# Kernel tuning notes

Hardware: AMD Instinct MI355X
Metric: run time of the kernel (lower is better)

## Reference

```python
import jax, jax.numpy as jnp
import numpy as np

N = 50000
E = 1600000
IN_F = 512
OUT_F = 128
NEG_SLOPE = 0.01   # nn.LeakyReLU() default
TEMPERATURE = 0.5


def setup_inputs() -> dict:
    key = jax.random.key(0)
    k1, k2, k3, k4 = jax.random.split(key, 4)
    h = jax.random.normal(k1, (N, IN_F), dtype=jnp.float32)
    # xavier_uniform with gain=1.414
    limW = 1.414 * np.sqrt(6.0 / (IN_F + OUT_F))
    W = jax.random.uniform(k2, (IN_F, OUT_F), minval=-limW, maxval=limW, dtype=jnp.float32)
    lima = 1.414 * np.sqrt(6.0 / (2 * OUT_F + 1))
    a = jax.random.uniform(k3, (2 * OUT_F, 1), minval=-lima, maxval=lima, dtype=jnp.float32)
    edge_index = jax.random.randint(k4, (2, E), 0, N, dtype=jnp.int64)
    return {"h": h, "W": W, "a": a, "edge_index": edge_index}


def reference(h, W, a, edge_index):
    # Inference: F.dropout(training=False) is identity.
    Wh = h @ W                                   # [N, F_out]
    src = edge_index[0]                          # row indices -> softmax segments
    dst = edge_index[1]
    # cat([Wh[src], Wh[dst]]) @ a == (Wh @ a1)[src] + (Wh @ a2)[dst]
    a1 = a[:OUT_F, 0]
    a2 = a[OUT_F:, 0]
    s1 = Wh @ a1                                 # [N]
    s2 = Wh @ a2                                 # [N]
    e = s1[src] + s2[dst]                        # [E]
    e = jnp.where(e >= 0, e, NEG_SLOPE * e)      # LeakyReLU
    logits = e / TEMPERATURE
    # sparse softmax over dim=1 (per source-node row segments)
    seg_max = jax.ops.segment_max(logits, src, num_segments=N)  # [N]
    ex = jnp.exp(logits - seg_max[src])          # [E]
    denom = jax.ops.segment_sum(ex, src, num_segments=N)        # [N]
    att = ex / denom[src]                        # [E]
    # sparse-dense matmul: h_prime[i] = sum_j att(i,j) * Wh[j]
    h_prime = jax.ops.segment_sum(att[:, None] * Wh[dst], src, num_segments=N)  # [N, F_out]
    return jax.nn.relu(h_prime)                  # concat=True path
```

## Files before the change

kernel.cpp:

```cpp
#include <hip/hip_runtime.h>
#include <cstdint>
#include <cstddef>

#define N_NODES 50000
#define N_EDGES 1600000
#define IN_FEAT 512
#define OUT_FEAT 128
#define NEG_SLOPE 0.01f
#define INV_TEMP 2.0f
#define PAD_DEG 128

#define BUCKETS 400
#define BNODES 125
#define BCAP 5000
#define A_BLOCKS 250
#define A_EPC (N_EDGES / A_BLOCKS)
#define A_G4 (A_EPC / 4)

#define CONV_BLOCKS ((IN_FEAT * OUT_FEAT) / 256)
#define GEMM_BLOCKS ((N_NODES + 63) / 64)

typedef __attribute__((ext_vector_type(8))) short short8;
typedef __attribute__((ext_vector_type(4))) float f32x4;

#define GLOBAL_AS __attribute__((address_space(1)))
#define LDS_AS __attribute__((address_space(3)))

__device__ inline unsigned short f2bf(float x) {
    unsigned int u = __float_as_uint(x);
    unsigned int r = (u + 0x7fffu + ((u >> 16) & 1u)) >> 16;
    return (unsigned short)r;
}
__device__ inline float bf2f(unsigned short b) {
    return __uint_as_float(((unsigned int)b) << 16);
}


__global__ __launch_bounds__(256) void build_kernel(const float* __restrict__ W,
                                                    unsigned short* __restrict__ Wt,
                                                    const int* __restrict__ src,
                                                    const int* __restrict__ dst,
                                                    int* __restrict__ bucket_cursor,
                                                    int* __restrict__ binned) {
    __shared__ int cntL[BUCKETS];
    __shared__ int baseL[BUCKETS];

    if (blockIdx.x >= A_BLOCKS) {
        int tid = (blockIdx.x - A_BLOCKS) * 256 + threadIdx.x;
        if (tid < IN_FEAT * OUT_FEAT) {
            int n = tid >> 9;
            int k = tid & 511;
            Wt[tid] = f2bf(W[k * OUT_FEAT + n]);
        }
        return;
    }

    int t = threadIdx.x;
    for (int i = t; i < BUCKETS; i += 256) cntL[i] = 0;
    __syncthreads();
    size_t ebase = (size_t)blockIdx.x * A_EPC;

    for (int g = t; g < A_G4; g += 256) {
        int4 s4 = *(const int4*)(src + ebase + (size_t)g * 4);
#pragma unroll
        for (int j = 0; j < 4; ++j) {
            int s = (&s4.x)[j];
            atomicAdd(&cntL[s / BNODES], 1);
        }
    }
    __syncthreads();
    for (int i = t; i < BUCKETS; i += 256) {
        int c = cntL[i];
        baseL[i] = c ? atomicAdd(&bucket_cursor[i], c) : 0;
        cntL[i] = 0;
    }
    __syncthreads();
    for (int g = t; g < A_G4; g += 256) {
        int4 s4 = *(const int4*)(src + ebase + (size_t)g * 4);
        int4 d4 = *(const int4*)(dst + ebase + (size_t)g * 4);
#pragma unroll
        for (int j = 0; j < 4; ++j) {
            int s = (&s4.x)[j];
            int b = s / BNODES;
            int sl = s - b * BNODES;
            int pos = atomicAdd(&cntL[b], 1);
            int slot = baseL[b] + pos;
            if (slot < BCAP)
                binned[(size_t)b * BCAP + slot] = (sl << 16) | (&d4.x)[j];
        }
    }
}


__global__ __launch_bounds__(256) void gemm_binB_kernel(const float* __restrict__ h,
                                                        const unsigned short* __restrict__ Wt,
                                                        const float* __restrict__ a_vec,
                                                        unsigned short* __restrict__ Whb,
                                                        float* __restrict__ s1,
                                                        float* __restrict__ s2,
                                                        const int* __restrict__ bucket_cursor,
                                                        const int* __restrict__ binned,
                                                        int* __restrict__ cnt,
                                                        int* __restrict__ csr) {
    __shared__ unsigned short lB[2][8 * 2 * 64 * 8];

    if (blockIdx.x < BUCKETS) {
        int* cL = (int*)&lB[0][0];
        int b = blockIdx.x;
        int t = threadIdx.x;
        if (t < BNODES) cL[t] = 0;
        __syncthreads();
        int m = min(bucket_cursor[b], BCAP);
        const int* bp = binned + (size_t)b * BCAP;
        int n0 = b * BNODES;
        for (int i = t; i < m; i += 256) {
            int p = bp[i];
            int sl = p >> 16;
            int d = p & 0xFFFF;
            int pos = atomicAdd(&cL[sl], 1);
            if (pos < PAD_DEG) csr[(size_t)(n0 + sl) * PAD_DEG + pos] = d;
        }
        __syncthreads();
        if (t < BNODES) cnt[n0 + t] = min(cL[t], PAD_DEG);
        return;
    }

    int bid = blockIdx.x - BUCKETS;
    int t = threadIdx.x;
    int w = t >> 6;
    int L = t & 63;
    int m0 = bid * 64;

    int arow = m0 + w * 16 + (L & 15);
    bool arow_ok = arow < N_NODES;
    int kq = (L >> 4) * 8;
    const float* arp = h + (size_t)arow * IN_FEAT + kq;

    f32x4 acc[8];
#pragma unroll
    for (int i = 0; i < 8; ++i) acc[i] = (f32x4){0.f, 0.f, 0.f, 0.f};

    auto stageB = [&](int buf, int k0) {
#pragma unroll
        for (int c = 0; c < 4; ++c) {
            int nb = w * 2 + (c >> 1);
            int ksub = c & 1;
            const GLOBAL_AS unsigned short* g =
                (const GLOBAL_AS unsigned short*)(Wt + (size_t)(nb * 16 + (L & 15)) * IN_FEAT +
                                                  (k0 + ksub * 32 + kq));
            LDS_AS unsigned short* lp = (LDS_AS unsigned short*)(&lB[buf][(nb * 2 + ksub) * 512]);
            __builtin_amdgcn_global_load_lds((const GLOBAL_AS void*)g, (LDS_AS void*)lp, 16, 0, 0);
        }
    };

    float4 av[2][2];
#pragma unroll
    for (int c = 0; c < 2; ++c) {
        av[c][0] = make_float4(0.f, 0.f, 0.f, 0.f);
        av[c][1] = make_float4(0.f, 0.f, 0.f, 0.f);
    }
    if (arow_ok) {
        av[0][0] = *(const float4*)(arp);
        av[0][1] = *(const float4*)(arp + 4);
        av[1][0] = *(const float4*)(arp + 32);
        av[1][1] = *(const float4*)(arp + 36);
    }
    stageB(0, 0);
    __syncthreads();

#pragma unroll
    for (int it = 0; it < 8; ++it) {
        const int buf = it & 1;

        if (it < 7) stageB(buf ^ 1, (it + 1) * 64);

        float4 avn[2][2];
#pragma unroll
        for (int c = 0; c < 2; ++c) {
            avn[c][0] = make_float4(0.f, 0.f, 0.f, 0.f);
            avn[c][1] = make_float4(0.f, 0.f, 0.f, 0.f);
        }
        if (it < 7 && arow_ok) {
            const float* p = arp + (it + 1) * 64;
            avn[0][0] = *(const float4*)(p);
            avn[0][1] = *(const float4*)(p + 4);
            avn[1][0] = *(const float4*)(p + 32);
            avn[1][1] = *(const float4*)(p + 36);
        }

        short8 af[2];
#pragma unroll
        for (int c = 0; c < 2; ++c) {
            short8 v;
            v[0] = (short)f2bf(av[c][0].x); v[1] = (short)f2bf(av[c][0].y);
            v[2] = (short)f2bf(av[c][0].z); v[3] = (short)f2bf(av[c][0].w);
            v[4] = (short)f2bf(av[c][1].x); v[5] = (short)f2bf(av[c][1].y);
            v[6] = (short)f2bf(av[c][1].z); v[7] = (short)f2bf(av[c][1].w);
            af[c] = v;
        }

#pragma unroll
        for (int ksub = 0; ksub < 2; ++ksub) {
#pragma unroll
            for (int nb = 0; nb < 8; ++nb) {
                short8 bf = *(const short8*)(&lB[buf][((nb * 2 + ksub) * 64 + L) * 8]);
                acc[nb] = __builtin_amdgcn_mfma_f32_16x16x32_bf16(af[ksub], bf, acc[nb], 0, 0, 0);
            }
        }

        __syncthreads();
#pragma unroll
        for (int c = 0; c < 2; ++c) {
            av[c][0] = avn[c][0];
            av[c][1] = avn[c][1];
        }
    }

    int col0 = L & 15;
    int rbase = m0 + w * 16 + (L >> 4) * 4;

    float a1c[8], a2c[8];
#pragma unroll
    for (int nb = 0; nb < 8; ++nb) {
        a1c[nb] = a_vec[nb * 16 + col0];
        a2c[nb] = a_vec[128 + nb * 16 + col0];
    }

#pragma unroll
    for (int r = 0; r < 4; ++r) {
        int row = rbase + r;
        bool ok = row < N_NODES;
        float p1 = 0.f, p2 = 0.f;
        if (ok) {
            unsigned short* orow = Whb + (size_t)row * OUT_FEAT;
#pragma unroll
            for (int nb = 0; nb < 8; ++nb) {
                float v = acc[nb][r];
                orow[nb * 16 + col0] = f2bf(v);
                p1 = fmaf(v, a1c[nb], p1);
                p2 = fmaf(v, a2c[nb], p2);
            }
        }
#pragma unroll
        for (int off = 8; off > 0; off >>= 1) {
            p1 += __shfl_xor(p1, off, 64);
            p2 += __shfl_xor(p2, off, 64);
        }
        if (ok && col0 == 0) {
            s1[row] = p1;
            s2[row] = p2;
        }
    }
}


__global__ __launch_bounds__(256) void node_kernel(const unsigned short* __restrict__ Whb,
                                                   const float* __restrict__ s1,
                                                   const float* __restrict__ s2,
                                                   const int* __restrict__ cnt,
                                                   const int* __restrict__ csr,
                                                   float* __restrict__ out) {
    int lane = threadIdx.x & 63;
    int w = threadIdx.x >> 6;
    int n = blockIdx.x * 4 + w;
    if (n >= N_NODES) return;
    int deg = cnt[n];
    size_t start = (size_t)n * PAD_DEG;
    int g = lane >> 4;
    int fo = lane & 15;

    float accv[8];
#pragma unroll
    for (int f = 0; f < 8; ++f) accv[f] = 0.f;
    float inv = 0.f;

    if (deg > 0) {
        float s1n = s1[n];
        int d0 = 0, d1 = 0;
        float ex0 = 0.f, ex1 = 0.f;
        if (lane < deg) {
            d0 = csr[start + lane];
            float ev = s1n + s2[d0];
            ev = ev >= 0.f ? ev : NEG_SLOPE * ev;
            ex0 = __expf(ev * INV_TEMP);
        }
        if (lane + 64 < deg) {
            d1 = csr[start + lane + 64];
            float ev = s1n + s2[d1];
            ev = ev >= 0.f ? ev : NEG_SLOPE * ev;
            ex1 = __expf(ev * INV_TEMP);
        }
        float denom = ex0 + ex1;
#pragma unroll
        for (int off = 32; off > 0; off >>= 1) denom += __shfl_xor(denom, off, 64);
        inv = 1.0f / denom;

#pragma unroll 2
        for (int jj = 0; jj < deg; jj += 4) {
            int e = jj + g;
            bool hi = jj >= 64;
            float exs = hi ? ex1 : ex0;
            int dsel = hi ? d1 : d0;
            float p = __shfl(exs, e & 63, 64);
            int dd = __shfl(dsel, e & 63, 64);
            short8 row = *(const short8*)(Whb + (size_t)dd * OUT_FEAT + fo * 8);
#pragma unroll
            for (int f = 0; f < 8; ++f)
                accv[f] = fmaf(p, bf2f((unsigned short)row[f]), accv[f]);
        }
#pragma unroll
        for (int f = 0; f < 8; ++f) {
            accv[f] += __shfl_xor(accv[f], 16, 64);
            accv[f] += __shfl_xor(accv[f], 32, 64);
        }
    }

    if (g == 0) {
        float* orow = out + (size_t)n * OUT_FEAT + fo * 8;
        float4 o0, o1;
        o0.x = fmaxf(accv[0] * inv, 0.f); o0.y = fmaxf(accv[1] * inv, 0.f);
        o0.z = fmaxf(accv[2] * inv, 0.f); o0.w = fmaxf(accv[3] * inv, 0.f);
        o1.x = fmaxf(accv[4] * inv, 0.f); o1.y = fmaxf(accv[5] * inv, 0.f);
        o1.z = fmaxf(accv[6] * inv, 0.f); o1.w = fmaxf(accv[7] * inv, 0.f);
        *(float4*)(orow) = o0;
        *(float4*)(orow + 4) = o1;
    }
}


extern "C" void kernel_launch(void* const* d_in, const int* in_sizes, int n_in,
                              void* d_out, int out_size, void* d_ws, size_t ws_size,
                              hipStream_t stream) {
    const float* h = (const float*)d_in[0];
    const float* W = (const float*)d_in[1];
    const float* a = (const float*)d_in[2];
    const int* edge = (const int*)d_in[3];
    const int* src = edge;
    const int* dst = edge + N_EDGES;
    float* out = (float*)d_out;

    char* ws = (char*)d_ws;
    size_t off = 0;
    auto alloc = [&](size_t bytes) -> void* {
        void* p = ws + off;
        off = (off + bytes + 255) & ~(size_t)255;
        return p;
    };
    unsigned short* Whb = (unsigned short*)alloc((size_t)N_NODES * OUT_FEAT * sizeof(unsigned short));
    float* s1 = (float*)alloc((size_t)N_NODES * sizeof(float));
    float* s2 = (float*)alloc((size_t)N_NODES * sizeof(float));
    int* cnt = (int*)alloc((size_t)N_NODES * sizeof(int));
    int* csr = (int*)alloc((size_t)N_NODES * PAD_DEG * sizeof(int));
    unsigned short* Wt = (unsigned short*)alloc((size_t)IN_FEAT * OUT_FEAT * sizeof(unsigned short));
    int* bucket_cursor = (int*)alloc((size_t)BUCKETS * sizeof(int));
    int* binned = (int*)alloc((size_t)BUCKETS * BCAP * sizeof(int));

    hipMemsetAsync(bucket_cursor, 0, BUCKETS * sizeof(int), stream);
    build_kernel<<<A_BLOCKS + CONV_BLOCKS, 256, 0, stream>>>(W, Wt, src, dst, bucket_cursor, binned);
    gemm_binB_kernel<<<BUCKETS + GEMM_BLOCKS, 256, 0, stream>>>(h, Wt, a, Whb, s1, s2,
                                                                bucket_cursor, binned, cnt, csr);
    node_kernel<<<(N_NODES + 3) / 4, 256, 0, stream>>>(Whb, s1, s2, cnt, csr, out);
}
```

Before: 262.8 us.

## Load GEMM B fragments directly to registers and double rows per wave

The GEMM part of the fused bin/gemm kernel no longer stages the bf16 weight tile into LDS through global_load_lds with double buffering and block barriers. Each wave now reads its B fragments straight from global memory (L2-resident, 128 KB) into registers and reuses them across two 16-row M tiles, so blocks cover 128 rows instead of 64. This removes the LDS traffic and the per-iteration __syncthreads and halves the GEMM block count. In exchange it raises register pressure (32 accumulators plus 16 B fragments) and repeats the global reads of W in every wave.

```diff
diff --git a/kernel.cpp b/kernel.cpp
--- a/kernel.cpp
+++ b/kernel.cpp
@@ -18,7 +18,7 @@
 #define A_G4 (A_EPC / 4)
 
 #define CONV_BLOCKS ((IN_FEAT * OUT_FEAT) / 256)
-#define GEMM_BLOCKS ((N_NODES + 63) / 64)
+#define GEMM_BLOCKS ((N_NODES + 127) / 128)
 
 typedef __attribute__((ext_vector_type(8))) short short8;
 typedef __attribute__((ext_vector_type(4))) float f32x4;
@@ -102,10 +102,9 @@
                                                         const int* __restrict__ binned,
                                                         int* __restrict__ cnt,
                                                         int* __restrict__ csr) {
-    __shared__ unsigned short lB[2][8 * 2 * 64 * 8];
+    __shared__ int cL[BNODES];
 
     if (blockIdx.x < BUCKETS) {
-        int* cL = (int*)&lB[0][0];
         int b = blockIdx.x;
         int t = threadIdx.x;
         if (t < BNODES) cL[t] = 0;
@@ -129,95 +128,109 @@
     int t = threadIdx.x;
     int w = t >> 6;
     int L = t & 63;
-    int m0 = bid * 64;
-
-    int arow = m0 + w * 16 + (L & 15);
-    bool arow_ok = arow < N_NODES;
+    int m0 = bid * 128;
+    int col0 = L & 15;
     int kq = (L >> 4) * 8;
-    const float* arp = h + (size_t)arow * IN_FEAT + kq;
-
-    f32x4 acc[8];
-#pragma unroll
-    for (int i = 0; i < 8; ++i) acc[i] = (f32x4){0.f, 0.f, 0.f, 0.f};
-
-    auto stageB = [&](int buf, int k0) {
-#pragma unroll
-        for (int c = 0; c < 4; ++c) {
-            int nb = w * 2 + (c >> 1);
-            int ksub = c & 1;
-            const GLOBAL_AS unsigned short* g =
-                (const GLOBAL_AS unsigned short*)(Wt + (size_t)(nb * 16 + (L & 15)) * IN_FEAT +
-                                                  (k0 + ksub * 32 + kq));
-            LDS_AS unsigned short* lp = (LDS_AS unsigned short*)(&lB[buf][(nb * 2 + ksub) * 512]);
-            __builtin_amdgcn_global_load_lds((const GLOBAL_AS void*)g, (LDS_AS void*)lp, 16, 0, 0);
-        }
-    };
-
-    float4 av[2][2];
-#pragma unroll
-    for (int c = 0; c < 2; ++c) {
-        av[c][0] = make_float4(0.f, 0.f, 0.f, 0.f);
-        av[c][1] = make_float4(0.f, 0.f, 0.f, 0.f);
-    }
-    if (arow_ok) {
-        av[0][0] = *(const float4*)(arp);
-        av[0][1] = *(const float4*)(arp + 4);
-        av[1][0] = *(const float4*)(arp + 32);
-        av[1][1] = *(const float4*)(arp + 36);
-    }
-    stageB(0, 0);
-    __syncthreads();
+
+    int arow[2];
+    bool arow_ok[2];
+    const float* arp[2];
+#pragma unroll
+    for (int m = 0; m < 2; ++m) {
+        arow[m] = m0 + w * 32 + m * 16 + col0;
+        arow_ok[m] = arow[m] < N_NODES;
+        arp[m] = h + (size_t)arow[m] * IN_FEAT + kq;
+    }
+
+    const unsigned short* bbase = Wt + (size_t)col0 * IN_FEAT + kq;
+
+    f32x4 acc[2][8];
+#pragma unroll
+    for (int m = 0; m < 2; ++m)
+#pragma unroll
+        for (int nb = 0; nb < 8; ++nb) acc[m][nb] = (f32x4){0.f, 0.f, 0.f, 0.f};
+
+    float4 av[2][2][2];
+#pragma unroll
+    for (int m = 0; m < 2; ++m)
+#pragma unroll
+        for (int c = 0; c < 2; ++c) {
+            av[m][c][0] = make_float4(0.f, 0.f, 0.f, 0.f);
+            av[m][c][1] = make_float4(0.f, 0.f, 0.f, 0.f);
+        }
+#pragma unroll
+    for (int m = 0; m < 2; ++m)
+        if (arow_ok[m]) {
+            av[m][0][0] = *(const float4*)(arp[m]);
+            av[m][0][1] = *(const float4*)(arp[m] + 4);
+            av[m][1][0] = *(const float4*)(arp[m] + 32);
+            av[m][1][1] = *(const float4*)(arp[m] + 36);
+        }
 
 #pragma unroll
     for (int it = 0; it < 8; ++it) {
-        const int buf = it & 1;
-
-        if (it < 7) stageB(buf ^ 1, (it + 1) * 64);
-
-        float4 avn[2][2];
-#pragma unroll
-        for (int c = 0; c < 2; ++c) {
-            avn[c][0] = make_float4(0.f, 0.f, 0.f, 0.f);
-            avn[c][1] = make_float4(0.f, 0.f, 0.f, 0.f);
-        }
-        if (it < 7 && arow_ok) {
-            const float* p = arp + (it + 1) * 64;
-            avn[0][0] = *(const float4*)(p);
-            avn[0][1] = *(const float4*)(p + 4);
-            avn[1][0] = *(const float4*)(p + 32);
-            avn[1][1] = *(const float4*)(p + 36);
-        }
-
-        short8 af[2];
-#pragma unroll
-        for (int c = 0; c < 2; ++c) {
-            short8 v;
-            v[0] = (short)f2bf(av[c][0].x); v[1] = (short)f2bf(av[c][0].y);
-            v[2] = (short)f2bf(av[c][0].z); v[3] = (short)f2bf(av[c][0].w);
-            v[4] = (short)f2bf(av[c][1].x); v[5] = (short)f2bf(av[c][1].y);
-            v[6] = (short)f2bf(av[c][1].z); v[7] = (short)f2bf(av[c][1].w);
-            af[c] = v;
-        }
-
-#pragma unroll
-        for (int ksub = 0; ksub < 2; ++ksub) {
+        const int k0 = it * 64;
+
+        float4 avn[2][2][2];
+#pragma unroll
+        for (int m = 0; m < 2; ++m)
+#pragma unroll
+            for (int c = 0; c < 2; ++c) {
+                avn[m][c][0] = make_float4(0.f, 0.f, 0.f, 0.f);
+                avn[m][c][1] = make_float4(0.f, 0.f, 0.f, 0.f);
+            }
+        if (it < 7) {
+#pragma unroll
+            for (int m = 0; m < 2; ++m)
+                if (arow_ok[m]) {
+                    const float* p = arp[m] + (it + 1) * 64;
+                    avn[m][0][0] = *(const float4*)(p);
+                    avn[m][0][1] = *(const float4*)(p + 4);
+                    avn[m][1][0] = *(const float4*)(p + 32);
+                    avn[m][1][1] = *(const float4*)(p + 36);
+                }
+        }
+
+        short8 bfr[2][8];
+#pragma unroll
+        for (int ksub = 0; ksub < 2; ++ksub)
+#pragma unroll
+            for (int nb = 0; nb < 8; ++nb)
+                bfr[ksub][nb] =
+                    *(const short8*)(bbase + (size_t)nb * 16 * IN_FEAT + k0 + ksub * 32);
+
+        short8 af[2][2];
+#pragma unroll
+        for (int m = 0; m < 2; ++m)
+#pragma unroll
+            for (int c = 0; c < 2; ++c) {
+                short8 v;
+                v[0] = (short)f2bf(av[m][c][0].x); v[1] = (short)f2bf(av[m][c][0].y);
+                v[2] = (short)f2bf(av[m][c][0].z); v[3] = (short)f2bf(av[m][c][0].w);
+                v[4] = (short)f2bf(av[m][c][1].x); v[5] = (short)f2bf(av[m][c][1].y);
+                v[6] = (short)f2bf(av[m][c][1].z); v[7] = (short)f2bf(av[m][c][1].w);
+                af[m][c] = v;
+            }
+
+#pragma unroll
+        for (int ksub = 0; ksub < 2; ++ksub)
 #pragma unroll
             for (int nb = 0; nb < 8; ++nb) {
-                short8 bf = *(const short8*)(&lB[buf][((nb * 2 + ksub) * 64 + L) * 8]);
-                acc[nb] = __builtin_amdgcn_mfma_f32_16x16x32_bf16(af[ksub], bf, acc[nb], 0, 0, 0);
-            }
-        }
-
-        __syncthreads();
-#pragma unroll
-        for (int c = 0; c < 2; ++c) {
-            av[c][0] = avn[c][0];
-            av[c][1] = avn[c][1];
-        }
-    }
-
-    int col0 = L & 15;
-    int rbase = m0 + w * 16 + (L >> 4) * 4;
+#pragma unroll
+                for (int m = 0; m < 2; ++m)
+                    acc[m][nb] = __builtin_amdgcn_mfma_f32_16x16x32_bf16(af[m][ksub],
+                                                                         bfr[ksub][nb],
+                                                                         acc[m][nb], 0, 0, 0);
+            }
+
+#pragma unroll
+        for (int m = 0; m < 2; ++m)
+#pragma unroll
+            for (int c = 0; c < 2; ++c) {
+                av[m][c][0] = avn[m][c][0];
+                av[m][c][1] = avn[m][c][1];
+            }
+    }
 
     float a1c[8], a2c[8];
 #pragma unroll
@@ -227,28 +240,32 @@
     }
 
 #pragma unroll
-    for (int r = 0; r < 4; ++r) {
-        int row = rbase + r;
-        bool ok = row < N_NODES;
-        float p1 = 0.f, p2 = 0.f;
-        if (ok) {
-            unsigned short* orow = Whb + (size_t)row * OUT_FEAT;
-#pragma unroll
-            for (int nb = 0; nb < 8; ++nb) {
-                float v = acc[nb][r];
-                orow[nb * 16 + col0] = f2bf(v);
-                p1 = fmaf(v, a1c[nb], p1);
-                p2 = fmaf(v, a2c[nb], p2);
-            }
-        }
-#pragma unroll
-        for (int off = 8; off > 0; off >>= 1) {
-            p1 += __shfl_xor(p1, off, 64);
-            p2 += __shfl_xor(p2, off, 64);
-        }
-        if (ok && col0 == 0) {
-            s1[row] = p1;
-            s2[row] = p2;
+    for (int m = 0; m < 2; ++m) {
+        int rbase = m0 + w * 32 + m * 16 + (L >> 4) * 4;
+#pragma unroll
+        for (int r = 0; r < 4; ++r) {
+            int row = rbase + r;
+            bool ok = row < N_NODES;
+            float p1 = 0.f, p2 = 0.f;
+            if (ok) {
+                unsigned short* orow = Whb + (size_t)row * OUT_FEAT;
+#pragma unroll
+                for (int nb = 0; nb < 8; ++nb) {
+                    float v = acc[m][nb][r];
+                    orow[nb * 16 + col0] = f2bf(v);
+                    p1 = fmaf(v, a1c[nb], p1);
+                    p2 = fmaf(v, a2c[nb], p2);
+                }
+            }
+#pragma unroll
+            for (int off = 8; off > 0; off >>= 1) {
+                p1 += __shfl_xor(p1, off, 64);
+                p2 += __shfl_xor(p2, off, 64);
+            }
+            if (ok && col0 == 0) {
+                s1[row] = p1;
+                s2[row] = p2;
+            }
         }
     }
 }
```

Measured after the change: 269.8 us. +2.7%, slower.

## Pre-convert h to bf16 in build kernel and load GEMM operands directly from global

Applied to the files above, without the earlier changes.

Adds a pass in the build kernel that converts h to a bf16 copy. The GEMM then reads bf16 A fragments directly and loads B fragments of Wt straight from global memory instead of staging them through LDS with barriers. The block order is swapped so GEMM blocks come before bucket blocks. This removes per-iteration conversion and synchronisation from the GEMM, but adds a full extra write and re-read of a bf16 copy of h.

```diff
diff --git a/kernel.cpp b/kernel.cpp
--- a/kernel.cpp
+++ b/kernel.cpp
@@ -18,6 +18,7 @@
 #define A_G4 (A_EPC / 4)
 
 #define CONV_BLOCKS ((IN_FEAT * OUT_FEAT) / 256)
+#define HCONV_BLOCKS ((N_NODES * IN_FEAT) / (256 * 8))
 #define GEMM_BLOCKS ((N_NODES + 63) / 64)
 
 typedef __attribute__((ext_vector_type(8))) short short8;
@@ -38,6 +39,8 @@
 
 __global__ __launch_bounds__(256) void build_kernel(const float* __restrict__ W,
                                                     unsigned short* __restrict__ Wt,
+                                                    const float* __restrict__ h,
+                                                    unsigned short* __restrict__ hb,
                                                     const int* __restrict__ src,
                                                     const int* __restrict__ dst,
                                                     int* __restrict__ bucket_cursor,
@@ -45,13 +48,26 @@
     __shared__ int cntL[BUCKETS];
     __shared__ int baseL[BUCKETS];
 
-    if (blockIdx.x >= A_BLOCKS) {
-        int tid = (blockIdx.x - A_BLOCKS) * 256 + threadIdx.x;
+    if (blockIdx.x >= A_BLOCKS + HCONV_BLOCKS) {
+        int tid = (blockIdx.x - A_BLOCKS - HCONV_BLOCKS) * 256 + threadIdx.x;
         if (tid < IN_FEAT * OUT_FEAT) {
             int n = tid >> 9;
             int k = tid & 511;
             Wt[tid] = f2bf(W[k * OUT_FEAT + n]);
         }
+        return;
+    }
+
+    if (blockIdx.x >= A_BLOCKS) {
+        size_t base = ((size_t)(blockIdx.x - A_BLOCKS) * 256 + threadIdx.x) * 8;
+        float4 v0 = *(const float4*)(h + base);
+        float4 v1 = *(const float4*)(h + base + 4);
+        short8 o;
+        o[0] = (short)f2bf(v0.x); o[1] = (short)f2bf(v0.y);
+        o[2] = (short)f2bf(v0.z); o[3] = (short)f2bf(v0.w);
+        o[4] = (short)f2bf(v1.x); o[5] = (short)f2bf(v1.y);
+        o[6] = (short)f2bf(v1.z); o[7] = (short)f2bf(v1.w);
+        *(short8*)(hb + base) = o;
         return;
     }
 
@@ -92,7 +108,7 @@
 }
 
 
-__global__ __launch_bounds__(256) void gemm_binB_kernel(const float* __restrict__ h,
+__global__ __launch_bounds__(256) void gemm_binB_kernel(const unsigned short* __restrict__ hb,
                                                         const unsigned short* __restrict__ Wt,
                                                         const float* __restrict__ a_vec,
                                                         unsigned short* __restrict__ Whb,
@@ -102,11 +118,10 @@
                                                         const int* __restrict__ binned,
                                                         int* __restrict__ cnt,
                                                         int* __restrict__ csr) {
-    __shared__ unsigned short lB[2][8 * 2 * 64 * 8];
-
-    if (blockIdx.x < BUCKETS) {
-        int* cL = (int*)&lB[0][0];
-        int b = blockIdx.x;
+    __shared__ int cL[BNODES];
+
+    if (blockIdx.x >= GEMM_BLOCKS) {
+        int b = blockIdx.x - GEMM_BLOCKS;
         int t = threadIdx.x;
         if (t < BNODES) cL[t] = 0;
         __syncthreads();
@@ -125,99 +140,62 @@
         return;
     }
 
-    int bid = blockIdx.x - BUCKETS;
+    int bid = blockIdx.x;
     int t = threadIdx.x;
     int w = t >> 6;
     int L = t & 63;
     int m0 = bid * 64;
-
-    int arow = m0 + w * 16 + (L & 15);
+    int col0 = L & 15;
+    int kq = (L >> 4) * 8;
+
+    int arow = m0 + w * 16 + col0;
     bool arow_ok = arow < N_NODES;
-    int kq = (L >> 4) * 8;
-    const float* arp = h + (size_t)arow * IN_FEAT + kq;
+    const unsigned short* hrow = hb + (size_t)arow * IN_FEAT;
+
+    const unsigned short* bbase = Wt + (size_t)col0 * IN_FEAT + kq;
 
     f32x4 acc[8];
 #pragma unroll
-    for (int i = 0; i < 8; ++i) acc[i] = (f32x4){0.f, 0.f, 0.f, 0.f};
-
-    auto stageB = [&](int buf, int k0) {
-#pragma unroll
-        for (int c = 0; c < 4; ++c) {
-            int nb = w * 2 + (c >> 1);
-            int ksub = c & 1;
-            const GLOBAL_AS unsigned short* g =
-                (const GLOBAL_AS unsigned short*)(Wt + (size_t)(nb * 16 + (L & 15)) * IN_FEAT +
-                                                  (k0 + ksub * 32 + kq));
-            LDS_AS unsigned short* lp = (LDS_AS unsigned short*)(&lB[buf][(nb * 2 + ksub) * 512]);
-            __builtin_amdgcn_global_load_lds((const GLOBAL_AS void*)g, (LDS_AS void*)lp, 16, 0, 0);
-        }
-    };
-
-    float4 av[2][2];
-#pragma unroll
-    for (int c = 0; c < 2; ++c) {
-        av[c][0] = make_float4(0.f, 0.f, 0.f, 0.f);
-        av[c][1] = make_float4(0.f, 0.f, 0.f, 0.f);
-    }
+    for (int nb = 0; nb < 8; ++nb) acc[nb] = (f32x4){0.f, 0.f, 0.f, 0.f};
+
+    short8 af[2];
+#pragma unroll
+    for (int c = 0; c < 2; ++c) af[c] = (short8){0, 0, 0, 0, 0, 0, 0, 0};
     if (arow_ok) {
-        av[0][0] = *(const float4*)(arp);
-        av[0][1] = *(const float4*)(arp + 4);
-        av[1][0] = *(const float4*)(arp + 32);
-        av[1][1] = *(const float4*)(arp + 36);
-    }
-    stageB(0, 0);
-    __syncthreads();
+        af[0] = *(const short8*)(hrow + kq);
+        af[1] = *(const short8*)(hrow + 32 + kq);
+    }
 
 #pragma unroll
     for (int it = 0; it < 8; ++it) {
-        const int buf = it & 1;
-
-        if (it < 7) stageB(buf ^ 1, (it + 1) * 64);
-
-        float4 avn[2][2];
-#pragma unroll
-        for (int c = 0; c < 2; ++c) {
-            avn[c][0] = make_float4(0.f, 0.f, 0.f, 0.f);
-            avn[c][1] = make_float4(0.f, 0.f, 0.f, 0.f);
-        }
+        const int k0 = it * 64;
+
+        short8 afn[2];
+#pragma unroll
+        for (int c = 0; c < 2; ++c) afn[c] = (short8){0, 0, 0, 0, 0, 0, 0, 0};
         if (it < 7 && arow_ok) {
-            const float* p = arp + (it + 1) * 64;
-            avn[0][0] = *(const float4*)(p);
-            avn[0][1] = *(const float4*)(p + 4);
-            avn[1][0] = *(const float4*)(p + 32);
-            avn[1][1] = *(const float4*)(p + 36);
-        }
-
-        short8 af[2];
-#pragma unroll
-        for (int c = 0; c < 2; ++c) {
-            short8 v;
-            v[0] = (short)f2bf(av[c][0].x); v[1] = (short)f2bf(av[c][0].y);
-            v[2] = (short)f2bf(av[c][0].z); v[3] = (short)f2bf(av[c][0].w);
-            v[4] = (short)f2bf(av[c][1].x); v[5] = (short)f2bf(av[c][1].y);
-            v[6] = (short)f2bf(av[c][1].z); v[7] = (short)f2bf(av[c][1].w);
-            af[c] = v;
-        }
-
-#pragma unroll
-        for (int ksub = 0; ksub < 2; ++ksub) {
-#pragma unroll
-            for (int nb = 0; nb < 8; ++nb) {
-                short8 bf = *(const short8*)(&lB[buf][((nb * 2 + ksub) * 64 + L) * 8]);
-                acc[nb] = __builtin_amdgcn_mfma_f32_16x16x32_bf16(af[ksub], bf, acc[nb], 0, 0, 0);
-            }
-        }
-
-        __syncthreads();
-#pragma unroll
-        for (int c = 0; c < 2; ++c) {
-            av[c][0] = avn[c][0];
-            av[c][1] = avn[c][1];
-        }
-    }
-
-    int col0 = L & 15;
-    int rbase = m0 + w * 16 + (L >> 4) * 4;
+            afn[0] = *(const short8*)(hrow + (it + 1) * 64 + kq);
+            afn[1] = *(const short8*)(hrow + (it + 1) * 64 + 32 + kq);
+        }
+
+        short8 bfr[2][8];
+#pragma unroll
+        for (int ksub = 0; ksub < 2; ++ksub)
+#pragma unroll
+            for (int nb = 0; nb < 8; ++nb)
+                bfr[ksub][nb] =
+                    *(const short8*)(bbase + (size_t)nb * 16 * IN_FEAT + k0 + ksub * 32);
+
+#pragma unroll
+        for (int ksub = 0; ksub < 2; ++ksub)
+#pragma unroll
+            for (int nb = 0; nb < 8; ++nb)
+                acc[nb] = __builtin_amdgcn_mfma_f32_16x16x32_bf16(af[ksub], bfr[ksub][nb],
+                                                                  acc[nb], 0, 0, 0);
+
+        af[0] = afn[0];
+        af[1] = afn[1];
+    }
 
     float a1c[8], a2c[8];
 #pragma unroll
@@ -226,6 +204,7 @@
         a2c[nb] = a_vec[128 + nb * 16 + col0];
     }
 
+    int rbase = m0 + w * 16 + (L >> 4) * 4;
 #pragma unroll
     for (int r = 0; r < 4; ++r) {
         int row = rbase + r;
@@ -352,12 +331,14 @@
     int* cnt = (int*)alloc((size_t)N_NODES * sizeof(int));
     int* csr = (int*)alloc((size_t)N_NODES * PAD_DEG * sizeof(int));
     unsigned short* Wt = (unsigned short*)alloc((size_t)IN_FEAT * OUT_FEAT * sizeof(unsigned short));
+    unsigned short* hb = (unsigned short*)alloc((size_t)N_NODES * IN_FEAT * sizeof(unsigned short));
     int* bucket_cursor = (int*)alloc((size_t)BUCKETS * sizeof(int));
     int* binned = (int*)alloc((size_t)BUCKETS * BCAP * sizeof(int));
 
     hipMemsetAsync(bucket_cursor, 0, BUCKETS * sizeof(int), stream);
-    build_kernel<<<A_BLOCKS + CONV_BLOCKS, 256, 0, stream>>>(W, Wt, src, dst, bucket_cursor, binned);
-    gemm_binB_kernel<<<BUCKETS + GEMM_BLOCKS, 256, 0, stream>>>(h, Wt, a, Whb, s1, s2,
+    build_kernel<<<A_BLOCKS + HCONV_BLOCKS + CONV_BLOCKS, 256, 0, stream>>>(
+        W, Wt, h, hb, src, dst, bucket_cursor, binned);
+    gemm_binB_kernel<<<GEMM_BLOCKS + BUCKETS, 256, 0, stream>>>(hb, Wt, a, Whb, s1, s2,
                                                                 bucket_cursor, binned, cnt, csr);
     node_kernel<<<(N_NODES + 3) / 4, 256, 0, stream>>>(Whb, s1, s2, cnt, csr, out);
 }
```

Result: slower. 309.3 us (+17.7%).
